# Kernel optimization log

Measured on AMD Instinct MI355X. Metric: run time of the kernel, lower is better.

Reference implementation:

```python
import jax, jax.numpy as jnp
import numpy as np
import math

D_MODEL = 1024
NHEAD = 16
HEAD_DIM = D_MODEL // NHEAD
ROPE_BASE = 10000.0


def _rope(x):
    # x: [B, H, S, Dh]; rotate per the RoPE class (half-split variant)
    d = x.shape[-1]
    half = d // 2
    seq_len = x.shape[2]
    theta = 1.0 / (ROPE_BASE ** (jnp.arange(0, d, 2, dtype=jnp.float32) / d))  # [d/2]
    ang = jnp.arange(seq_len, dtype=jnp.float32)[:, None] * theta[None, :]      # [S, d/2]
    ang2 = jnp.concatenate([ang, ang], axis=-1)                                 # [S, d]
    cos_ = jnp.cos(ang2)[None, None, :, :]
    sin_ = jnp.sin(ang2)[None, None, :, :]
    neg_half = jnp.concatenate([-x[..., half:], x[..., :half]], axis=-1)
    return x * cos_ + neg_half * sin_


def setup_inputs() -> dict:
    key = jax.random.key(0)
    ks = jax.random.split(key, 10)
    B, S, D = 4, 2048, D_MODEL
    scale = 1.0 / math.sqrt(D)
    x = jax.random.normal(ks[0], (B, S, D), dtype=jnp.float32)
    Wq = jax.random.normal(ks[1], (D, D), dtype=jnp.float32) * scale
    bq = jnp.zeros((D,), dtype=jnp.float32)
    Wk = jax.random.normal(ks[2], (D, D), dtype=jnp.float32) * scale
    bk = jnp.zeros((D,), dtype=jnp.float32)
    Wv = jax.random.normal(ks[3], (D, D), dtype=jnp.float32) * scale
    bv = jnp.zeros((D,), dtype=jnp.float32)
    Wo = jax.random.normal(ks[4], (D, D), dtype=jnp.float32) * scale
    bo = jnp.zeros((D,), dtype=jnp.float32)
    # causal mask: mask==1 means masked (upper triangle)
    mask = jnp.triu(jnp.ones((S, S), dtype=jnp.int32), k=1)[None, None, :, :]
    return {"x": x, "Wq": Wq, "bq": bq, "Wk": Wk, "bk": bk,
            "Wv": Wv, "bv": bv, "Wo": Wo, "bo": bo, "mask": mask}


def reference(x, Wq, bq, Wk, bk, Wv, bv, Wo, bo, mask):
    B, S, D = x.shape
    H, Dh = NHEAD, HEAD_DIM

    def proj(W, b):
        y = jnp.einsum('bsd,ed->bse', x, W) + b  # torch Linear: x @ W.T + b
        return y.reshape(B, S, H, Dh).transpose(0, 2, 1, 3)  # [B,H,S,Dh]

    q = _rope(proj(Wq, bq))
    k = _rope(proj(Wk, bk))
    v = proj(Wv, bv)

    a = jnp.einsum('bhqd,bhkd->bhqk', q, k) / math.sqrt(Dh)  # [B,H,S,S]
    a = jnp.where(mask == 1, jnp.float32(-1e9), a)
    a = jax.nn.softmax(a, axis=-1)
    out = jnp.einsum('bhqk,bhkd->bhqd', a, v)                 # [B,H,S,Dh]
    out = out.transpose(0, 2, 1, 3).reshape(B, S, D)
    return jnp.einsum('bsd,ed->bse', out, Wo) + bo
```

## Files before the change

### kernel.cpp

```cpp
#include <hip/hip_runtime.h>
#include <stdint.h>

typedef unsigned short u16;
typedef __bf16 bf16x8 __attribute__((ext_vector_type(8)));
typedef __bf16 bf16x2 __attribute__((ext_vector_type(2)));
typedef float f32x4 __attribute__((ext_vector_type(4)));
typedef float f32x16 __attribute__((ext_vector_type(16)));

#define SEQ    2048
#define NHEAD  16
#define DH     64
#define DMODEL 1024
#define NBH    64

__device__ __forceinline__ u16 cvt1(float f){
  union { __bf16 h; u16 u; } c; c.h = (__bf16)f; return c.u;
}
__device__ __forceinline__ uint32_t cvt2(float a, float b){
  union { bf16x2 v; uint32_t u; } c; c.v = bf16x2{(__bf16)a, (__bf16)b}; return c.u;
}
__device__ __forceinline__ int swz(int row){ return (((row&7)^((row>>3)&7))<<4); }

typedef const __attribute__((address_space(1))) uint32_t* gas_t;
typedef __attribute__((address_space(3))) uint32_t* las_t;
__device__ __forceinline__ void async16(const void* g, void* l){
  __builtin_amdgcn_global_load_lds((gas_t)g, (las_t)l, 16, 0, 0);
}

__global__ void prep(const float* __restrict__ x,  const float* __restrict__ Wq,
                     const float* __restrict__ Wk, const float* __restrict__ Wv,
                     const float* __restrict__ Wo,
                     u16* __restrict__ xb, u16* __restrict__ wqkv,
                     u16* __restrict__ wob, float* __restrict__ tab)
{
  const int bid = blockIdx.x, tid = threadIdx.x;
  if (bid < 6144){
    const float* src; u16* dst; int lb;
    if      (bid < 4096){ src = x;  dst = xb;              lb = bid; }
    else if (bid < 4608){ src = Wq; dst = wqkv;            lb = bid-4096; }
    else if (bid < 5120){ src = Wk; dst = wqkv + 1048576;  lb = bid-4608; }
    else if (bid < 5632){ src = Wv; dst = wqkv + 2097152;  lb = bid-5120; }
    else                { src = Wo; dst = wob;             lb = bid-5632; }
    const size_t off = (size_t)lb*2048 + tid*8;
    float4 a = *(const float4*)(src+off);
    float4 b = *(const float4*)(src+off+4);
    bf16x8 o = { (__bf16)a.x,(__bf16)a.y,(__bf16)a.z,(__bf16)a.w,
                 (__bf16)b.x,(__bf16)b.y,(__bf16)b.z,(__bf16)b.w };
    *(bf16x8*)(dst+off) = o;
  } else {
    const int t = (bid-6144)*256 + tid;
    const int s = t >> 5, j = t & 31;
    double freq = exp(-(double)(2*j)/64.0*log(10000.0));
    double ang = (double)s*freq;
    tab[s*64 + 2*j]     = (float)cos(ang);
    tab[s*64 + 2*j + 1] = (float)sin(ang);
  }
}

template<int MODE>
__global__ __launch_bounds__(256, 2)
void gemm_bt(const u16* __restrict__ A, const u16* __restrict__ W,
             const float* __restrict__ b0, const float* __restrict__ b1,
             const float* __restrict__ b2, float* __restrict__ fout,
             u16* __restrict__ dq, u16* __restrict__ dk, u16* __restrict__ dv,
             const float* __restrict__ tab)
{
  __shared__ u16 Ab[128*32];
  __shared__ u16 Bb[128*32];
  const int tid = threadIdx.x;
  const int lane = tid & 63;
  const int w = tid >> 6, wr = w >> 1, wc = w & 1;
  const int m0 = blockIdx.y * 128;
  const int n0 = blockIdx.x * 128;
  const int c0 = lane & 15, g = lane >> 4;

  f32x4 acc[4][4] = {};

  const int sr = tid >> 2;
  const int sc = (tid & 3) * 8;
  const u16* ga = A + (size_t)(m0 + sr) * DMODEL + sc;
  const u16* gb = W + (size_t)(n0 + sr) * DMODEL + sc;
  u16* la = Ab + sr*32 + sc;
  u16* lb = Bb + sr*32 + sc;

  for (int k0 = 0; k0 < DMODEL; k0 += 32) {
    __syncthreads();
    async16(ga + k0,             la);
    async16(ga + k0 + 64*DMODEL, la + 64*32);
    async16(gb + k0,             lb);
    async16(gb + k0 + 64*DMODEL, lb + 64*32);
    __syncthreads();
    bf16x8 afr[4], bfr[4];
#pragma unroll
    for (int i=0;i<4;i++) afr[i] = *(const bf16x8*)(Ab + (wr*64 + i*16 + c0)*32 + g*8);
#pragma unroll
    for (int j=0;j<4;j++) bfr[j] = *(const bf16x8*)(Bb + (wc*64 + j*16 + c0)*32 + g*8);
    __builtin_amdgcn_s_setprio(1);
#pragma unroll
    for (int i=0;i<4;i++)
#pragma unroll
      for (int j=0;j<4;j++)
        acc[i][j] = __builtin_amdgcn_mfma_f32_16x16x32_bf16(afr[i], bfr[j], acc[i][j], 0,0,0);
    __builtin_amdgcn_s_setprio(0);
  }

  const int nbase = n0 + wc*64;
  const int t = n0 >> 10;
  const float* bias = (MODE==1) ? b0 : (t==0) ? b0 : (t==1) ? b1 : b2;
  float bv4[4];
#pragma unroll
  for (int j=0;j<4;j++) bv4[j] = bias[(nbase & 1023) + j*16 + c0];

  if (MODE == 0) {
    u16* dst = (t==0) ? dq : (t==1) ? dk : dv;
    const float qs = (t==0) ? 0.18033688011f : 1.0f;
    const int h = (nbase >> 6) & (NHEAD-1);
#pragma unroll
    for (int i=0;i<4;i++){
      const int mbase = m0 + wr*64 + i*16 + g*4;
#pragma unroll
      for (int r=0;r<4;r++){
        const int mm = mbase + r;
        const int bb = mm >> 11, s = mm & (SEQ-1);
        const size_t rowbase = (((size_t)(bb*NHEAD + h))*SEQ + s)*DH;
        if (t < 2) {
#pragma unroll
          for (int j2=0;j2<2;j2++){
            const int dh = j2*16 + c0;
            const float xl = acc[i][j2][r]   + bv4[j2];
            const float xh = acc[i][j2+2][r] + bv4[j2+2];
            const float2 cs = *(const float2*)(tab + (size_t)s*64 + dh*2);
            dst[rowbase + dh]      = cvt1((xl*cs.x - xh*cs.y)*qs);
            dst[rowbase + dh + 32] = cvt1((xh*cs.x + xl*cs.y)*qs);
          }
        } else {
#pragma unroll
          for (int j=0;j<4;j++)
            dst[rowbase + j*16 + c0] = cvt1(acc[i][j][r] + bv4[j]);
        }
      }
    }
  } else {
#pragma unroll
    for (int i=0;i<4;i++){
      const int mbase = m0 + wr*64 + i*16 + g*4;
#pragma unroll
      for (int j=0;j<4;j++){
#pragma unroll
        for (int r=0;r<4;r++)
          fout[(size_t)(mbase + r) * DMODEL + nbase + j*16 + c0] = acc[i][j][r] + bv4[j];
      }
    }
  }
}

__global__ __launch_bounds__(256, 2)
void attn_fwd(const u16* __restrict__ Q, const u16* __restrict__ K,
              const u16* __restrict__ V, u16* __restrict__ O)
{
  __shared__ u16 Kb[2][64*64];
  __shared__ u16 Vt[2][64*64];
  const int bh = blockIdx.x;
  const int pair = blockIdx.y;
  const int tid = threadIdx.x, lane = tid & 63, w = tid >> 6;
  const int c31 = lane & 31, hi = lane >> 5;
  const size_t hb = (size_t)bh * SEQ * DH;
  const int b = bh >> 4, h = bh & 15;

  const int boff1 = tid*16;
  const int ksw1  = boff1 ^ swz(boff1 >> 7);
  const int boff2 = boff1 + 4096;
  const int ksw2  = boff2 ^ swz(boff2 >> 7);
  const int rp = tid >> 3, dc = tid & 7;
  const int kv0 = 2*rp;
  const int vpos = (kv0 & 0x33) | ((kv0 & 4) << 1) | ((kv0 & 8) >> 1);
  union U4 { ushort4 v; u16 e[4]; };

#pragma unroll 1
  for (int half = 0; half < 2; half++){
    const int qt = half ? (15 - pair) : pair;
    const int qrow_base = qt*128 + w*32;
    const int jt_last  = 2*qt + 1;
    const int jt_end_w = 2*qt + (w>>1);
    const int q = qrow_base + c31;

    bf16x8 qf[4];
#pragma unroll
    for (int kc=0;kc<4;kc++)
      qf[kc] = *(const bf16x8*)(Q + hb + (size_t)q*DH + kc*16 + hi*8);

    f32x16 oacc0 = {}, oacc1 = {};
    float mrun = -3.0e38f, lrun = 0.f;

    {
      const char* gk = (const char*)(K + hb);
      async16(gk + ksw1, (char*)Kb[0] + boff1);
      async16(gk + ksw2, (char*)Kb[0] + boff2);
      const u16* gv = V + hb;
      U4 v0a, v0b, v1a, v1b;
      v0a.v = *(const ushort4*)(gv + (kv0  )*DH + dc*8);
      v0b.v = *(const ushort4*)(gv + (kv0  )*DH + dc*8 + 4);
      v1a.v = *(const ushort4*)(gv + (kv0+1)*DH + dc*8);
      v1b.v = *(const ushort4*)(gv + (kv0+1)*DH + dc*8 + 4);
#pragma unroll
      for (int e=0;e<8;e++){
        const int row = dc*8 + e;
        const u16 a   = (e<4) ? v0a.e[e] : v0b.e[e-4];
        const u16 bb2 = (e<4) ? v1a.e[e] : v1b.e[e-4];
        *(uint32_t*)((char*)Vt[0] + ((row*128 + vpos*2) ^ swz(row))) =
          (uint32_t)a | ((uint32_t)bb2 << 16);
      }
    }
    __syncthreads();

    U4 v0a, v0b, v1a, v1b;
    for (int jt = 0; jt <= jt_last; jt++){
      const int cur = jt & 1, nxt = cur ^ 1;
      const bool pre = (jt < jt_last);
      if (pre){
        const char* gk = (const char*)(K + hb + (size_t)(jt+1)*64*DH);
        async16(gk + ksw1, (char*)Kb[nxt] + boff1);
        async16(gk + ksw2, (char*)Kb[nxt] + boff2);
        const u16* gv = V + hb + (size_t)(jt+1)*64*DH;
        v0a.v = *(const ushort4*)(gv + (kv0  )*DH + dc*8);
        v0b.v = *(const ushort4*)(gv + (kv0  )*DH + dc*8 + 4);
        v1a.v = *(const ushort4*)(gv + (kv0+1)*DH + dc*8);
        v1b.v = *(const ushort4*)(gv + (kv0+1)*DH + dc*8 + 4);
      }

      if (jt <= jt_end_w){
        f32x16 sT[2] = {};
#pragma unroll
        for (int kc=0;kc<4;kc++){
          const int col = (kc*16 + hi*8)*2;
          const int r0 = c31, r1 = 32 + c31;
          const bf16x8 kf0 = *(const bf16x8*)((const char*)Kb[cur] + ((r0*128 + col) ^ swz(r0)));
          const bf16x8 kf1 = *(const bf16x8*)((const char*)Kb[cur] + ((r1*128 + col) ^ swz(r1)));
          __builtin_amdgcn_s_setprio(1);
          sT[0] = __builtin_amdgcn_mfma_f32_32x32x16_bf16(kf0, qf[kc], sT[0], 0,0,0);
          sT[1] = __builtin_amdgcn_mfma_f32_32x32x16_bf16(kf1, qf[kc], sT[1], 0,0,0);
          __builtin_amdgcn_s_setprio(0);
        }
        if (jt == jt_end_w){
#pragma unroll
          for (int kvb=0;kvb<2;kvb++)
#pragma unroll
            for (int r=0;r<16;r++){
              const int kv = jt*64 + kvb*32 + (r&3) + 8*(r>>2) + 4*hi;
              sT[kvb][r] = (kv <= q) ? sT[kvb][r] : -3.0e38f;
            }
        }
        float mx = -3.0e38f;
#pragma unroll
        for (int kvb=0;kvb<2;kvb++)
#pragma unroll
          for (int r=0;r<16;r++) mx = fmaxf(mx, sT[kvb][r]);
        mx = fmaxf(mx, __shfl_xor(mx, 32));
        const bool grow = __any(mx > mrun + 8.0f);
        float corr = 1.0f;
        if (grow){
          const float mnew = fmaxf(mrun, mx);
          corr = exp2f(mrun - mnew);
          mrun = mnew;
        }
        float lsum = 0.f;
#pragma unroll
        for (int kvb=0;kvb<2;kvb++)
#pragma unroll
          for (int r=0;r<16;r++){
            const float p = exp2f(sT[kvb][r] - mrun);
            sT[kvb][r] = p;
            lsum += p;
          }
        lsum += __shfl_xor(lsum, 32);
        lrun = lrun*corr + lsum;
        if (grow){
#pragma unroll
          for (int r=0;r<16;r++){ oacc0[r] *= corr; oacc1[r] *= corr; }
        }
#pragma unroll
        for (int kvb=0;kvb<2;kvb++)
#pragma unroll
          for (int s=0;s<2;s++){
            union { bf16x8 v; uint32_t d[4]; } pa;
#pragma unroll
            for (int j=0;j<4;j++)
              pa.d[j] = cvt2(sT[kvb][s*8+2*j], sT[kvb][s*8+2*j+1]);
            const int col = (kvb*32 + s*16 + hi*8)*2;
            const int r0 = c31, r1 = 32 + c31;
            const bf16x8 vf0 = *(const bf16x8*)((const char*)Vt[cur] + ((r0*128 + col) ^ swz(r0)));
            const bf16x8 vf1 = *(const bf16x8*)((const char*)Vt[cur] + ((r1*128 + col) ^ swz(r1)));
            __builtin_amdgcn_s_setprio(1);
            oacc0 = __builtin_amdgcn_mfma_f32_32x32x16_bf16(vf0, pa.v, oacc0, 0,0,0);
            oacc1 = __builtin_amdgcn_mfma_f32_32x32x16_bf16(vf1, pa.v, oacc1, 0,0,0);
            __builtin_amdgcn_s_setprio(0);
          }
      }

      if (pre){
#pragma unroll
        for (int e=0;e<8;e++){
          const int row = dc*8 + e;
          const u16 a   = (e<4) ? v0a.e[e] : v0b.e[e-4];
          const u16 bb2 = (e<4) ? v1a.e[e] : v1b.e[e-4];
          *(uint32_t*)((char*)Vt[nxt] + ((row*128 + vpos*2) ^ swz(row))) =
            (uint32_t)a | ((uint32_t)bb2 << 16);
        }
      }
      __syncthreads();
    }

    {
      const float inv = 1.0f / lrun;
      u16* orow = O + ((size_t)b*SEQ + q)*DMODEL + h*DH;
#pragma unroll
      for (int r2=0;r2<8;r2++){
        const int dh0 = 2*(r2&1) + 8*(r2>>1) + 4*hi;
        *(uint32_t*)(orow + dh0)      = cvt2(oacc0[2*r2]*inv, oacc0[2*r2+1]*inv);
        *(uint32_t*)(orow + 32 + dh0) = cvt2(oacc1[2*r2]*inv, oacc1[2*r2+1]*inv);
      }
    }
  }
}

extern "C" void kernel_launch(void* const* d_in, const int* in_sizes, int n_in,
                              void* d_out, int out_size, void* d_ws, size_t ws_size,
                              hipStream_t stream)
{
  const float* x  = (const float*)d_in[0];
  const float* Wq = (const float*)d_in[1];
  const float* bq = (const float*)d_in[2];
  const float* Wk = (const float*)d_in[3];
  const float* bk = (const float*)d_in[4];
  const float* Wv = (const float*)d_in[5];
  const float* bv = (const float*)d_in[6];
  const float* Wo = (const float*)d_in[7];
  const float* bo = (const float*)d_in[8];

  const size_t MB = 1024*1024;
  char* ws = (char*)d_ws;
  u16*  xb   = (u16*)(ws);
  u16*  aw   = (u16*)(ws);
  u16*  vw   = (u16*)(ws + 16*MB);
  u16*  wqkv = (u16*)(ws + 32*MB);
  u16*  wob  = (u16*)(ws + 38*MB);
  float* tab = (float*)(ws + 41*MB);
  u16*  qw = (u16*)d_out;
  u16*  kw = (u16*)d_out + 8*MB;

  prep<<<dim3(6400), dim3(256), 0, stream>>>(x, Wq, Wk, Wv, Wo, xb, wqkv, wob, tab);

  gemm_bt<0><<<dim3(24, 64), dim3(256), 0, stream>>>(xb, wqkv, bq, bk, bv,
                                                     nullptr, qw, kw, vw, tab);

  attn_fwd<<<dim3(64, 8), dim3(256), 0, stream>>>(qw, kw, vw, aw);

  gemm_bt<1><<<dim3(8, 64), dim3(256), 0, stream>>>(aw, wob, bo, nullptr, nullptr,
                                                    (float*)d_out, nullptr, nullptr, nullptr, nullptr);
}
```

Baseline: 192.3 us.

## Double-buffer GEMM LDS tiles and tighten attention softmax and V transpose

```diff
diff --git a/kernel.cpp b/kernel.cpp
--- a/kernel.cpp
+++ b/kernel.cpp
@@ -21,10 +21,38 @@
 }
 __device__ __forceinline__ int swz(int row){ return (((row&7)^((row>>3)&7))<<4); }
 
+#if __has_builtin(__builtin_amdgcn_exp2f)
+__device__ __forceinline__ float EXP2(float x){ return __builtin_amdgcn_exp2f(x); }
+#else
+__device__ __forceinline__ float EXP2(float x){ return exp2f(x); }
+#endif
+__device__ __forceinline__ float max3f(float a, float b, float c){
+  float r; asm("v_max3_f32 %0, %1, %2, %3" : "=v"(r) : "v"(a), "v"(b), "v"(c));
+  return r;
+}
+
 typedef const __attribute__((address_space(1))) uint32_t* gas_t;
 typedef __attribute__((address_space(3))) uint32_t* las_t;
 __device__ __forceinline__ void async16(const void* g, void* l){
   __builtin_amdgcn_global_load_lds((gas_t)g, (las_t)l, 16, 0, 0);
+}
+
+__device__ __forceinline__ void vstore8(char* dst, uint2 a0, uint2 a1,
+                                        uint2 b0, uint2 b1, int dc, int vpos){
+  uint32_t pk[8];
+  pk[0] = __builtin_amdgcn_perm(b0.x, a0.x, 0x05040100u);
+  pk[1] = __builtin_amdgcn_perm(b0.x, a0.x, 0x07060302u);
+  pk[2] = __builtin_amdgcn_perm(b0.y, a0.y, 0x05040100u);
+  pk[3] = __builtin_amdgcn_perm(b0.y, a0.y, 0x07060302u);
+  pk[4] = __builtin_amdgcn_perm(b1.x, a1.x, 0x05040100u);
+  pk[5] = __builtin_amdgcn_perm(b1.x, a1.x, 0x07060302u);
+  pk[6] = __builtin_amdgcn_perm(b1.y, a1.y, 0x05040100u);
+  pk[7] = __builtin_amdgcn_perm(b1.y, a1.y, 0x07060302u);
+#pragma unroll
+  for (int e=0;e<8;e++){
+    const int row = dc*8 + e;
+    *(uint32_t*)(dst + ((row*128 + vpos*2) ^ swz(row))) = pk[e];
+  }
 }
 
 __global__ void prep(const float* __restrict__ x,  const float* __restrict__ Wq,
@@ -65,8 +93,8 @@
              u16* __restrict__ dq, u16* __restrict__ dk, u16* __restrict__ dv,
              const float* __restrict__ tab)
 {
-  __shared__ u16 Ab[128*32];
-  __shared__ u16 Bb[128*32];
+  __shared__ u16 Ab[2][128*32];
+  __shared__ u16 Bb[2][128*32];
   const int tid = threadIdx.x;
   const int lane = tid & 63;
   const int w = tid >> 6, wr = w >> 1, wc = w & 1;
@@ -78,23 +106,29 @@
 
   const int sr = tid >> 2;
   const int sc = (tid & 3) * 8;
+  const int stoff = sr*32 + sc;
   const u16* ga = A + (size_t)(m0 + sr) * DMODEL + sc;
   const u16* gb = W + (size_t)(n0 + sr) * DMODEL + sc;
-  u16* la = Ab + sr*32 + sc;
-  u16* lb = Bb + sr*32 + sc;
-
+
+#define STAGE_G(buf, kk) do{ \
+    async16(ga + (kk),             Ab[buf] + stoff); \
+    async16(ga + (kk) + 64*DMODEL, Ab[buf] + stoff + 64*32); \
+    async16(gb + (kk),             Bb[buf] + stoff); \
+    async16(gb + (kk) + 64*DMODEL, Bb[buf] + stoff + 64*32); \
+  }while(0)
+
+  STAGE_G(0, 0);
+  __syncthreads();
+
+#pragma unroll 2
   for (int k0 = 0; k0 < DMODEL; k0 += 32) {
-    __syncthreads();
-    async16(ga + k0,             la);
-    async16(ga + k0 + 64*DMODEL, la + 64*32);
-    async16(gb + k0,             lb);
-    async16(gb + k0 + 64*DMODEL, lb + 64*32);
-    __syncthreads();
+    const int cur = (k0 >> 5) & 1;
+    if (k0 + 32 < DMODEL) STAGE_G(cur^1, k0 + 32);
     bf16x8 afr[4], bfr[4];
 #pragma unroll
-    for (int i=0;i<4;i++) afr[i] = *(const bf16x8*)(Ab + (wr*64 + i*16 + c0)*32 + g*8);
-#pragma unroll
-    for (int j=0;j<4;j++) bfr[j] = *(const bf16x8*)(Bb + (wc*64 + j*16 + c0)*32 + g*8);
+    for (int i=0;i<4;i++) afr[i] = *(const bf16x8*)(Ab[cur] + (wr*64 + i*16 + c0)*32 + g*8);
+#pragma unroll
+    for (int j=0;j<4;j++) bfr[j] = *(const bf16x8*)(Bb[cur] + (wc*64 + j*16 + c0)*32 + g*8);
     __builtin_amdgcn_s_setprio(1);
 #pragma unroll
     for (int i=0;i<4;i++)
@@ -102,7 +136,9 @@
       for (int j=0;j<4;j++)
         acc[i][j] = __builtin_amdgcn_mfma_f32_16x16x32_bf16(afr[i], bfr[j], acc[i][j], 0,0,0);
     __builtin_amdgcn_s_setprio(0);
-  }
+    __syncthreads();
+  }
+#undef STAGE_G
 
   const int nbase = n0 + wc*64;
   const int t = n0 >> 10;
@@ -174,7 +210,6 @@
   const int rp = tid >> 3, dc = tid & 7;
   const int kv0 = 2*rp;
   const int vpos = (kv0 & 0x33) | ((kv0 & 4) << 1) | ((kv0 & 8) >> 1);
-  union U4 { ushort4 v; u16 e[4]; };
 
 #pragma unroll 1
   for (int half = 0; half < 2; half++){
@@ -197,23 +232,15 @@
       async16(gk + ksw1, (char*)Kb[0] + boff1);
       async16(gk + ksw2, (char*)Kb[0] + boff2);
       const u16* gv = V + hb;
-      U4 v0a, v0b, v1a, v1b;
-      v0a.v = *(const ushort4*)(gv + (kv0  )*DH + dc*8);
-      v0b.v = *(const ushort4*)(gv + (kv0  )*DH + dc*8 + 4);
-      v1a.v = *(const ushort4*)(gv + (kv0+1)*DH + dc*8);
-      v1b.v = *(const ushort4*)(gv + (kv0+1)*DH + dc*8 + 4);
-#pragma unroll
-      for (int e=0;e<8;e++){
-        const int row = dc*8 + e;
-        const u16 a   = (e<4) ? v0a.e[e] : v0b.e[e-4];
-        const u16 bb2 = (e<4) ? v1a.e[e] : v1b.e[e-4];
-        *(uint32_t*)((char*)Vt[0] + ((row*128 + vpos*2) ^ swz(row))) =
-          (uint32_t)a | ((uint32_t)bb2 << 16);
-      }
+      uint2 a0 = *(const uint2*)(gv + (kv0  )*DH + dc*8);
+      uint2 a1 = *(const uint2*)(gv + (kv0  )*DH + dc*8 + 4);
+      uint2 b0 = *(const uint2*)(gv + (kv0+1)*DH + dc*8);
+      uint2 b1 = *(const uint2*)(gv + (kv0+1)*DH + dc*8 + 4);
+      vstore8((char*)Vt[0], a0, a1, b0, b1, dc, vpos);
     }
     __syncthreads();
 
-    U4 v0a, v0b, v1a, v1b;
+    uint2 pa0, pa1, pb0, pb1;
     for (int jt = 0; jt <= jt_last; jt++){
       const int cur = jt & 1, nxt = cur ^ 1;
       const bool pre = (jt < jt_last);
@@ -222,10 +249,10 @@
         async16(gk + ksw1, (char*)Kb[nxt] + boff1);
         async16(gk + ksw2, (char*)Kb[nxt] + boff2);
         const u16* gv = V + hb + (size_t)(jt+1)*64*DH;
-        v0a.v = *(const ushort4*)(gv + (kv0  )*DH + dc*8);
-        v0b.v = *(const ushort4*)(gv + (kv0  )*DH + dc*8 + 4);
-        v1a.v = *(const ushort4*)(gv + (kv0+1)*DH + dc*8);
-        v1b.v = *(const ushort4*)(gv + (kv0+1)*DH + dc*8 + 4);
+        pa0 = *(const uint2*)(gv + (kv0  )*DH + dc*8);
+        pa1 = *(const uint2*)(gv + (kv0  )*DH + dc*8 + 4);
+        pb0 = *(const uint2*)(gv + (kv0+1)*DH + dc*8);
+        pb1 = *(const uint2*)(gv + (kv0+1)*DH + dc*8 + 4);
       }
 
       if (jt <= jt_end_w){
@@ -250,28 +277,31 @@
               sT[kvb][r] = (kv <= q) ? sT[kvb][r] : -3.0e38f;
             }
         }
-        float mx = -3.0e38f;
-#pragma unroll
-        for (int kvb=0;kvb<2;kvb++)
-#pragma unroll
-          for (int r=0;r<16;r++) mx = fmaxf(mx, sT[kvb][r]);
+        float mx0 = -3.0e38f, mx1 = -3.0e38f;
+#pragma unroll
+        for (int r=0;r<16;r+=2){
+          mx0 = max3f(mx0, sT[0][r], sT[0][r+1]);
+          mx1 = max3f(mx1, sT[1][r], sT[1][r+1]);
+        }
+        float mx = fmaxf(mx0, mx1);
         mx = fmaxf(mx, __shfl_xor(mx, 32));
         const bool grow = __any(mx > mrun + 8.0f);
         float corr = 1.0f;
         if (grow){
           const float mnew = fmaxf(mrun, mx);
-          corr = exp2f(mrun - mnew);
+          corr = EXP2(mrun - mnew);
           mrun = mnew;
         }
-        float lsum = 0.f;
+        float ls[4] = {0.f, 0.f, 0.f, 0.f};
 #pragma unroll
         for (int kvb=0;kvb<2;kvb++)
 #pragma unroll
           for (int r=0;r<16;r++){
-            const float p = exp2f(sT[kvb][r] - mrun);
+            const float p = EXP2(sT[kvb][r] - mrun);
             sT[kvb][r] = p;
-            lsum += p;
+            ls[r & 3] += p;
           }
+        float lsum = (ls[0] + ls[1]) + (ls[2] + ls[3]);
         lsum += __shfl_xor(lsum, 32);
         lrun = lrun*corr + lsum;
         if (grow){
@@ -297,16 +327,7 @@
           }
       }
 
-      if (pre){
-#pragma unroll
-        for (int e=0;e<8;e++){
-          const int row = dc*8 + e;
-          const u16 a   = (e<4) ? v0a.e[e] : v0b.e[e-4];
-          const u16 bb2 = (e<4) ? v1a.e[e] : v1b.e[e-4];
-          *(uint32_t*)((char*)Vt[nxt] + ((row*128 + vpos*2) ^ swz(row))) =
-            (uint32_t)a | ((uint32_t)bb2 << 16);
-        }
-      }
+      if (pre) vstore8((char*)Vt[nxt], pa0, pa1, pb0, pb1, dc, vpos);
       __syncthreads();
     }
 
```

After: 176.0 us. -8.5%, faster.
